# Performance work log

Measured on AMD Instinct MI355X. Metric: run time of the kernel, lower is better.

The kernel has to match this reference:

```python
import jax, jax.numpy as jnp
import numpy as np

IN_FEATURES = 4096
OUT_FEATURES = 4096
BLOCK_SIZE = 64
BLOCK_NUM = 64
N_FACTORS = 3  # boft_n_butterfly_factor


def _butterfly_perm(n, b, r):
    # Mirrors BOFTLayer.block_butterfly_perm for n_butterfly_factor != 0.
    block_size = n // b
    step = block_size // r
    evens = np.arange(0, step, 2)
    odds = np.arange(1, step, 2)
    seq = np.concatenate([evens, odds])
    sorted_order = np.concatenate([np.arange(p * r, p * r + r) for p in seq])
    return np.arange(n).reshape(-1, block_size)[:, sorted_order].reshape(-1)


def setup_inputs() -> dict:
    key = jax.random.key(0)
    k1, k2, k3, k4, k5 = jax.random.split(key, 5)
    x = jax.random.normal(k1, (8, 2048, IN_FEATURES), dtype=jnp.float32)
    weight = jax.random.normal(k2, (OUT_FEATURES, IN_FEATURES), dtype=jnp.float32) * 0.02
    bias = jax.random.normal(k3, (OUT_FEATURES,), dtype=jnp.float32) * 0.02
    boft_R = jax.random.normal(k4, (N_FACTORS, BLOCK_NUM, BLOCK_SIZE, BLOCK_SIZE), dtype=jnp.float32) * 0.1
    boft_s = jax.random.uniform(k5, (OUT_FEATURES, 1), dtype=jnp.float32, minval=0.5, maxval=1.5)
    perm = jnp.asarray(np.stack([
        _butterfly_perm(IN_FEATURES, BLOCK_NUM // (2 ** i), BLOCK_SIZE // 2)
        for i in range(N_FACTORS)
    ]), dtype=jnp.int32)
    return {"x": x, "weight": weight, "bias": bias, "boft_R": boft_R,
            "boft_s": boft_s, "perm": perm}


def _cayley(R):
    # Q = (I - skew) @ inv(I + skew), skew = (R - R^T)/2; batched.
    skew = 0.5 * (R - jnp.swapaxes(R, -1, -2))
    I = jnp.eye(R.shape[-1], dtype=R.dtype)
    # Right-division via solve: X (I+skew) = (I-skew)
    Xt = jnp.linalg.solve(jnp.swapaxes(I + skew, -1, -2), jnp.swapaxes(I - skew, -1, -2))
    return jnp.swapaxes(Xt, -1, -2)


def _block_diag(blocks):
    # (D, H, H) -> (D*H, D*H) block-diagonal
    D, H, _ = blocks.shape
    out = jnp.zeros((D, H, D, H), blocks.dtype)
    out = out.at[jnp.arange(D), :, jnp.arange(D), :].set(blocks)
    return out.reshape(D * H, D * H)


def reference(x, weight, bias, boft_R, boft_s, perm):
    N, D, H, _ = boft_R.shape
    Q = _cayley(boft_R.reshape(N * D, H, H)).reshape(N, D, H, H)
    # P_i @ block_diag_i @ P_i^T implemented as a symmetric gather (P is a permutation)
    rot = None
    for i in range(N):  # small fixed loop over butterfly factors
        bd = _block_diag(Q[i])
        p = perm[i]
        mat = bd[p][:, p]  # (in, in)
        rot = mat if rot is None else mat @ rot
    # rotated_weight = (rot @ W^T)^T = W @ rot^T ; then scale rows by boft_s
    scaled_w = (weight @ rot.T) * boft_s  # (out, in)
    return x @ scaled_w.T + bias
```

## Files before the change

kernel.cpp:

```cpp
#include <hip/hip_runtime.h>
#include <hip/hip_bf16.h>
#include <cstddef>
#include <cstdint>

#define IN_F 4096
#define OUT_F 4096

typedef __attribute__((ext_vector_type(8))) _Float16 half8;
typedef __attribute__((ext_vector_type(4))) float f32x4;

__global__ __launch_bounds__(256) void cayley_kernel(const float* __restrict__ R,
                                                     float* __restrict__ Qs) {
  __shared__ float Mm[64][65];
  __shared__ float Bm[64][65];
  const int b = blockIdx.x;
  const float* Rb = R + (size_t)b * 4096;
  const int t = threadIdx.x;
  const int i = t >> 2;
  const int jb = (t & 3) << 4;

  #pragma unroll 4
  for (int q = 0; q < 16; ++q) {
    int j = jb + q;
    float rij = Rb[i * 64 + j];
    float rji = Rb[j * 64 + i];
    float sk = 0.5f * (rij - rji);
    float id = (i == j) ? 1.0f : 0.0f;
    Mm[i][j] = id - sk;
    Bm[i][j] = id + sk;
  }
  __syncthreads();

  for (int k = 0; k < 64; ++k) {
    float inv = 1.0f / Mm[k][k];
    float f = Mm[i][k];
    __syncthreads();
    if (t < 64) {
      Mm[k][t] *= inv;
      Bm[k][t] *= inv;
    }
    __syncthreads();
    if (i != k) {
      #pragma unroll 4
      for (int q = 0; q < 16; ++q) {
        int j = jb + q;
        Mm[i][j] = fmaf(-f, Mm[k][j], Mm[i][j]);
        Bm[i][j] = fmaf(-f, Bm[k][j], Bm[i][j]);
      }
    }
    __syncthreads();
  }

  float* out = Qs + (size_t)b * 4096;
  #pragma unroll 4
  for (int q = 0; q < 16; ++q) {
    int flat = t * 16 + q;
    out[flat] = Bm[flat >> 6][flat & 63];
  }
}

__global__ void invperm_kernel(const int* __restrict__ perm,
                               int* __restrict__ ip1, int* __restrict__ ip2) {
  int c = blockIdx.x * 256 + threadIdx.x;
  ip1[perm[4096 + c]] = c;
  ip2[perm[8192 + c]] = c;
}

__global__ void compose_kernel(const int* __restrict__ perm,
                               const int* __restrict__ ip1,
                               const int* __restrict__ ip2,
                               int* __restrict__ rho1, int* __restrict__ rho2) {
  int k = blockIdx.x * 256 + threadIdx.x;
  rho1[k] = perm[ip1[k]];
  rho2[k] = perm[4096 + ip2[k]];
}

__global__ __launch_bounds__(256) void transpose_perm_kernel(const float* __restrict__ W,
                                                             const int* __restrict__ p0,
                                                             float* __restrict__ U0) {
  __shared__ float tile[64][65];
  const int c0 = blockIdx.x * 64;
  const int n0 = blockIdx.y * 64;
  const int t = threadIdx.x;
  const int r = t >> 2;
  const int cb = (t & 3) << 4;
  #pragma unroll
  for (int q = 0; q < 4; ++q) {
    float4 v = *(const float4*)(W + (size_t)(n0 + r) * IN_F + c0 + cb + q * 4);
    tile[r][cb + q * 4 + 0] = v.x;
    tile[r][cb + q * 4 + 1] = v.y;
    tile[r][cb + q * 4 + 2] = v.z;
    tile[r][cb + q * 4 + 3] = v.w;
  }
  __syncthreads();
  const int c = t >> 2;
  const int nb = (t & 3) << 4;
  const int dstrow = p0[c0 + c];
  #pragma unroll
  for (int q = 0; q < 4; ++q) {
    float4 v;
    v.x = tile[nb + q * 4 + 0][c];
    v.y = tile[nb + q * 4 + 1][c];
    v.z = tile[nb + q * 4 + 2][c];
    v.w = tile[nb + q * 4 + 3][c];
    *(float4*)(U0 + (size_t)dstrow * OUT_F + n0 + nb + q * 4) = v;
  }
}

__global__ __launch_bounds__(256) void factor_kernel(const float* __restrict__ src,
                                                     float* __restrict__ dst,
                                                     const float* __restrict__ Qt,
                                                     const int* __restrict__ rowIdx,
                                                     const int* __restrict__ dstIdx,
                                                     const float* __restrict__ s) {
  __shared__ float qt[64][64];
  __shared__ int sidx[64];
  __shared__ int didx[64];
  const int g = blockIdx.y;
  const int n0 = blockIdx.x * 256;
  const int t = threadIdx.x;

  {
    const float* qg = Qt + (size_t)g * 4096;
    float4* qv = (float4*)&qt[0][0];
    #pragma unroll
    for (int q = 0; q < 4; ++q)
      qv[t * 4 + q] = *(const float4*)(qg + t * 16 + q * 4);
  }
  if (t < 64) {
    sidx[t] = rowIdx ? rowIdx[g * 64 + t] : g * 64 + t;
    didx[t] = dstIdx ? dstIdx[g * 64 + t] : g * 64 + t;
  }
  __syncthreads();

  const int w = t >> 6;
  const int lane = t & 63;
  const int nOff = n0 + lane * 4;
  float4 a[16];
  #pragma unroll
  for (int ii = 0; ii < 16; ++ii) a[ii] = make_float4(0.f, 0.f, 0.f, 0.f);

  for (int j = 0; j < 64; ++j) {
    float4 v = *(const float4*)(src + (size_t)sidx[j] * OUT_F + nOff);
    const float* qr = &qt[j][w * 16];
    #pragma unroll
    for (int ii = 0; ii < 16; ++ii) {
      float qq = qr[ii];
      a[ii].x = fmaf(qq, v.x, a[ii].x);
      a[ii].y = fmaf(qq, v.y, a[ii].y);
      a[ii].z = fmaf(qq, v.z, a[ii].z);
      a[ii].w = fmaf(qq, v.w, a[ii].w);
    }
  }

  float4 sv = make_float4(1.f, 1.f, 1.f, 1.f);
  if (s) sv = *(const float4*)(s + nOff);
  #pragma unroll
  for (int ii = 0; ii < 16; ++ii) {
    int r = didx[w * 16 + ii];
    float4 o;
    o.x = a[ii].x * sv.x; o.y = a[ii].y * sv.y;
    o.z = a[ii].z * sv.z; o.w = a[ii].w * sv.w;
    *(float4*)(dst + (size_t)r * OUT_F + nOff) = o;
  }
}

__global__ __launch_bounds__(256) void transpose_cvt_swz(const float* __restrict__ S,
                                                         _Float16* __restrict__ D) {
  __shared__ float tile[64][65];
  const int k0 = blockIdx.x * 64;
  const int n0 = blockIdx.y * 64;
  const int t = threadIdx.x;
  const int r = t >> 2;
  const int cb = (t & 3) << 4;
  #pragma unroll
  for (int q = 0; q < 4; ++q) {
    float4 v = *(const float4*)(S + (size_t)(k0 + r) * OUT_F + n0 + cb + q * 4);
    tile[r][cb + q * 4 + 0] = v.x;
    tile[r][cb + q * 4 + 1] = v.y;
    tile[r][cb + q * 4 + 2] = v.z;
    tile[r][cb + q * 4 + 3] = v.w;
  }
  __syncthreads();
  const int n = t >> 2;
  const int kb = (t & 3) << 4;
  half8 h0, h1;
  #pragma unroll
  for (int q = 0; q < 8; ++q) {
    h0[q] = (_Float16)tile[kb + q][n];
    h1[q] = (_Float16)tile[kb + 8 + q][n];
  }
  const int gn = n0 + n;
  const int sw = gn & 3;
  const int c0 = (k0 + kb) >> 3;
  const int c0s = (c0 & ~3) | ((c0 & 3) ^ sw);
  const int c1s = (c0 & ~3) | (((c0 + 1) & 3) ^ sw);
  _Float16* dp = D + (size_t)gn * IN_F;
  *(half8*)(dp + c0s * 8) = h0;
  *(half8*)(dp + c1s * 8) = h1;
}

__global__ __launch_bounds__(256) void cvt_x_kernel(const float* __restrict__ X,
                                                    _Float16* __restrict__ Ah) {
  const int idx = blockIdx.x * 256 + threadIdx.x;
  const int m = idx >> 9;
  const int c = idx & 511;
  const float* xp = X + (size_t)m * IN_F + c * 8;
  f32x4 v0 = *(const f32x4*)xp;
  f32x4 v1 = *(const f32x4*)(xp + 4);
  half8 h;
  h[0] = (_Float16)v0.x; h[1] = (_Float16)v0.y;
  h[2] = (_Float16)v0.z; h[3] = (_Float16)v0.w;
  h[4] = (_Float16)v1.x; h[5] = (_Float16)v1.y;
  h[6] = (_Float16)v1.z; h[7] = (_Float16)v1.w;
  const int cs = (c & ~3) | ((c & 3) ^ (m & 3));
  *(half8*)(Ah + (size_t)m * IN_F + cs * 8) = h;
}

#define TM 256
#define TN 256
#define TK 32
#define NSLOT 4

typedef const __attribute__((address_space(1))) uint32_t* gptr_t;
typedef __attribute__((address_space(3))) uint32_t* lptr_t;

#define WB(n) asm volatile("s_waitcnt vmcnt(" #n ")\ns_barrier" ::: "memory")

__global__ __launch_bounds__(512, 2) void mfma_gemm2(const _Float16* __restrict__ A,
                                                     const _Float16* __restrict__ B,
                                                     const float* __restrict__ bias,
                                                     float* __restrict__ C, int M) {
  __shared__ __align__(16) _Float16 lds[NSLOT][2][TM * TK];
  const int t = threadIdx.x;
  const int lane = t & 63;
  const int w = t >> 6;
  const int wr = w >> 2;
  const int wc = w & 3;

  const int nwg = gridDim.x * gridDim.y;
  const int lin = blockIdx.y * gridDim.x + blockIdx.x;
  const int cpx = nwg >> 3;
  const int nl = (lin & 7) * cpx + (lin >> 3);
  const int n0 = (nl & 15) * TN;
  const int m0 = (nl >> 4) * TM;

  const _Float16* gA[2];
  const _Float16* gB[2];
  int ldsoff[2];
  #pragma unroll
  for (int p = 0; p < 2; ++p) {
    int chunk = p * 512 + t;
    int row = chunk >> 2;
    int c = chunk & 3;
    gA[p] = A + (size_t)(m0 + row) * IN_F + c * 8;
    gB[p] = B + (size_t)(n0 + row) * IN_F + c * 8;
    ldsoff[p] = (p * 512 + (t & ~63)) * 8;
  }

  const int frow = lane & 15;
  const int kc = lane >> 4;
  int aoff[8], boff[4];
  #pragma unroll
  for (int i = 0; i < 8; ++i) {
    int r = wr * 128 + i * 16 + frow;
    aoff[i] = r * TK + ((kc ^ (r & 3)) << 3);
  }
  #pragma unroll
  for (int j = 0; j < 4; ++j) {
    int r = wc * 64 + j * 16 + frow;
    boff[j] = r * TK + ((kc ^ (r & 3)) << 3);
  }

  f32x4 acc[8][4];
  #pragma unroll
  for (int i = 0; i < 8; ++i)
    #pragma unroll
    for (int j = 0; j < 4; ++j) acc[i][j] = (f32x4){0.f, 0.f, 0.f, 0.f};

#define STAGE(tt, ss)                                                          \
  do {                                                                         \
    _Float16* sA = &lds[ss][0][0];                                             \
    _Float16* sB = &lds[ss][1][0];                                             \
    _Pragma("unroll") for (int p = 0; p < 2; ++p) {                            \
      __builtin_amdgcn_global_load_lds((gptr_t)(gA[p] + (tt) * TK),            \
                                       (lptr_t)(sA + ldsoff[p]), 16, 0, 0);    \
      __builtin_amdgcn_global_load_lds((gptr_t)(gB[p] + (tt) * TK),            \
                                       (lptr_t)(sB + ldsoff[p]), 16, 0, 0);    \
    }                                                                          \
  } while (0)

#define COMPUTE(ss)                                                            \
  do {                                                                         \
    const _Float16* As = &lds[ss][0][0];                                       \
    const _Float16* Bs = &lds[ss][1][0];                                       \
    half8 af[8], bf[4];                                                        \
    _Pragma("unroll") for (int i = 0; i < 8; ++i)                              \
        af[i] = *(const half8*)(As + aoff[i]);                                 \
    _Pragma("unroll") for (int j = 0; j < 4; ++j)                              \
        bf[j] = *(const half8*)(Bs + boff[j]);                                 \
    __builtin_amdgcn_s_setprio(1);                                             \
    _Pragma("unroll") for (int i = 0; i < 8; ++i)                              \
      _Pragma("unroll") for (int j = 0; j < 4; ++j)                            \
          acc[i][j] = __builtin_amdgcn_mfma_f32_16x16x32_f16(af[i], bf[j],     \
                                                             acc[i][j], 0, 0, 0); \
    __builtin_amdgcn_s_setprio(0);                                             \
  } while (0)

  STAGE(0, 0);
  STAGE(1, 1);
  STAGE(2, 2);
  WB(8);
  for (int tt = 0; tt < 125; ++tt) {
    STAGE(tt + 3, (tt + 3) & 3);
    COMPUTE(tt & 3);
    WB(8);
  }
  COMPUTE(1); WB(4);
  COMPUTE(2); WB(0);
  COMPUTE(3);

  const int crow = (lane >> 4) << 2;
  const int ccol = lane & 15;
  #pragma unroll
  for (int j = 0; j < 4; ++j) {
    int n = n0 + wc * 64 + j * 16 + ccol;
    float bv = bias[n];
    #pragma unroll
    for (int i = 0; i < 8; ++i) {
      int mbase = m0 + wr * 128 + i * 16 + crow;
      #pragma unroll
      for (int r = 0; r < 4; ++r)
        C[(size_t)(mbase + r) * OUT_F + n] = acc[i][j][r] + bv;
    }
  }
#undef STAGE
#undef COMPUTE
}

extern "C" void kernel_launch(void* const* d_in, const int* in_sizes, int n_in,
                              void* d_out, int out_size, void* d_ws, size_t ws_size,
                              hipStream_t stream) {
  const float* x      = (const float*)d_in[0];
  const float* weight = (const float*)d_in[1];
  const float* bias   = (const float*)d_in[2];
  const float* boft_R = (const float*)d_in[3];
  const float* boft_s = (const float*)d_in[4];
  const int*   perm   = (const int*)d_in[5];
  float* out = (float*)d_out;

  float* ws   = (float*)d_ws;
  float* Qs   = ws;
  float* bufA = ws + 786432;
  float* bufB = bufA + 16777216;
  _Float16* Bh = (_Float16*)(bufB + 16777216);
  int*   ints = (int*)(Bh + 16777216);
  int* ip1  = ints;
  int* ip2  = ints + 4096;
  int* rho1 = ints + 8192;
  int* rho2 = ints + 12288;
  _Float16* Ah = (_Float16*)bufA;

  const int M = in_sizes[0] / IN_F;

  hipLaunchKernelGGL(cayley_kernel, dim3(192), dim3(256), 0, stream, boft_R, Qs);
  hipLaunchKernelGGL(invperm_kernel, dim3(16), dim3(256), 0, stream, perm, ip1, ip2);
  hipLaunchKernelGGL(compose_kernel, dim3(16), dim3(256), 0, stream, perm, ip1, ip2, rho1, rho2);
  hipLaunchKernelGGL(transpose_perm_kernel, dim3(64, 64), dim3(256), 0, stream,
                     weight, perm, bufA);
  hipLaunchKernelGGL(factor_kernel, dim3(16, 64), dim3(256), 0, stream,
                     bufA, bufB, Qs, (const int*)nullptr, (const int*)nullptr,
                     (const float*)nullptr);
  hipLaunchKernelGGL(factor_kernel, dim3(16, 64), dim3(256), 0, stream,
                     bufB, bufA, Qs + 262144, rho1, (const int*)nullptr,
                     (const float*)nullptr);
  hipLaunchKernelGGL(factor_kernel, dim3(16, 64), dim3(256), 0, stream,
                     bufA, bufB, Qs + 524288, rho2, ip2, boft_s);
  hipLaunchKernelGGL(transpose_cvt_swz, dim3(64, 64), dim3(256), 0, stream,
                     bufB, Bh);
  hipLaunchKernelGGL(cvt_x_kernel, dim3((M * IN_F / 8) / 256), dim3(256), 0, stream,
                     x, Ah);
  hipLaunchKernelGGL(mfma_gemm2, dim3(OUT_F / TN, M / TM), dim3(512), 0, stream,
                     Ah, Bh, bias, out, M);
}
```

Measured before the change: 1.195 ms.

## Split GEMM K-step into two ping-pong phases and change LDS swizzle

Splits each K-tile's compute in the fp16 MFMA GEMM into two phases. Each phase issues part of the LDS fragment loads and half of the next tile's global-to-LDS prefetch (A, then B), then meets at a barrier before its MFMAs run at raised priority. This is meant to interleave memory and matrix work across waves, ping-pong style. It also changes the XOR swizzle key from row&3 to (row>>2)&3, consistently in the converters and the GEMM fragment offsets, to reduce LDS bank conflicts. The extra barriers per tile add synchronization cost, and overlapping STAGE writes with reads of other slots depends on the 4-slot ring staying correct.

```diff
diff --git a/kernel.cpp b/kernel.cpp
--- a/kernel.cpp
+++ b/kernel.cpp
@@ -191,7 +191,7 @@
     h1[q] = (_Float16)tile[kb + 8 + q][n];
   }
   const int gn = n0 + n;
-  const int sw = gn & 3;
+  const int sw = (gn >> 2) & 3;
   const int c0 = (k0 + kb) >> 3;
   const int c0s = (c0 & ~3) | ((c0 & 3) ^ sw);
   const int c1s = (c0 & ~3) | (((c0 + 1) & 3) ^ sw);
@@ -213,7 +213,7 @@
   h[2] = (_Float16)v0.z; h[3] = (_Float16)v0.w;
   h[4] = (_Float16)v1.x; h[5] = (_Float16)v1.y;
   h[6] = (_Float16)v1.z; h[7] = (_Float16)v1.w;
-  const int cs = (c & ~3) | ((c & 3) ^ (m & 3));
+  const int cs = (c & ~3) | ((c & 3) ^ ((m >> 2) & 3));
   *(half8*)(Ah + (size_t)m * IN_F + cs * 8) = h;
 }
 
@@ -225,7 +225,9 @@
 typedef const __attribute__((address_space(1))) uint32_t* gptr_t;
 typedef __attribute__((address_space(3))) uint32_t* lptr_t;
 
-#define WB(n) asm volatile("s_waitcnt vmcnt(" #n ")\ns_barrier" ::: "memory")
+#define BARRIER()  asm volatile("s_barrier" ::: "memory")
+#define LGKM0()    asm volatile("s_waitcnt lgkmcnt(0)" ::: "memory")
+#define TILE_END(n) asm volatile("s_waitcnt vmcnt(" #n ")\n\ts_barrier" ::: "memory")
 
 __global__ __launch_bounds__(512, 2) void mfma_gemm2(const _Float16* __restrict__ A,
                                                      const _Float16* __restrict__ B,
@@ -264,12 +266,12 @@
   #pragma unroll
   for (int i = 0; i < 8; ++i) {
     int r = wr * 128 + i * 16 + frow;
-    aoff[i] = r * TK + ((kc ^ (r & 3)) << 3);
+    aoff[i] = r * TK + ((kc ^ ((r >> 2) & 3)) << 3);
   }
   #pragma unroll
   for (int j = 0; j < 4; ++j) {
     int r = wc * 64 + j * 16 + frow;
-    boff[j] = r * TK + ((kc ^ (r & 3)) << 3);
+    boff[j] = r * TK + ((kc ^ ((r >> 2) & 3)) << 3);
   }
 
   f32x4 acc[8][4];
@@ -278,47 +280,74 @@
     #pragma unroll
     for (int j = 0; j < 4; ++j) acc[i][j] = (f32x4){0.f, 0.f, 0.f, 0.f};
 
-#define STAGE(tt, ss)                                                          \
+  half8 af[8], bf[4];
+
+#define STAGE_A(tt, ss)                                                        \
   do {                                                                         \
     _Float16* sA = &lds[ss][0][0];                                             \
-    _Float16* sB = &lds[ss][1][0];                                             \
-    _Pragma("unroll") for (int p = 0; p < 2; ++p) {                            \
+    _Pragma("unroll") for (int p = 0; p < 2; ++p)                              \
       __builtin_amdgcn_global_load_lds((gptr_t)(gA[p] + (tt) * TK),            \
                                        (lptr_t)(sA + ldsoff[p]), 16, 0, 0);    \
+  } while (0)
+
+#define STAGE_B(tt, ss)                                                        \
+  do {                                                                         \
+    _Float16* sB = &lds[ss][1][0];                                             \
+    _Pragma("unroll") for (int p = 0; p < 2; ++p)                              \
       __builtin_amdgcn_global_load_lds((gptr_t)(gB[p] + (tt) * TK),            \
                                        (lptr_t)(sB + ldsoff[p]), 16, 0, 0);    \
-    }                                                                          \
   } while (0)
 
-#define COMPUTE(ss)                                                            \
+#define PHASE1(ss, DOSTAGE, tt3)                                               \
   do {                                                                         \
     const _Float16* As = &lds[ss][0][0];                                       \
     const _Float16* Bs = &lds[ss][1][0];                                       \
-    half8 af[8], bf[4];                                                        \
-    _Pragma("unroll") for (int i = 0; i < 8; ++i)                              \
+    _Pragma("unroll") for (int i = 0; i < 4; ++i)                              \
         af[i] = *(const half8*)(As + aoff[i]);                                 \
     _Pragma("unroll") for (int j = 0; j < 4; ++j)                              \
         bf[j] = *(const half8*)(Bs + boff[j]);                                 \
+    if (DOSTAGE) STAGE_A(tt3, (tt3) & 3);                                      \
+    BARRIER();                                                                 \
+    LGKM0();                                                                   \
+    __builtin_amdgcn_sched_barrier(0);                                         \
     __builtin_amdgcn_s_setprio(1);                                             \
-    _Pragma("unroll") for (int i = 0; i < 8; ++i)                              \
+    _Pragma("unroll") for (int i = 0; i < 4; ++i)                              \
       _Pragma("unroll") for (int j = 0; j < 4; ++j)                            \
           acc[i][j] = __builtin_amdgcn_mfma_f32_16x16x32_f16(af[i], bf[j],     \
                                                              acc[i][j], 0, 0, 0); \
     __builtin_amdgcn_s_setprio(0);                                             \
+    BARRIER();                                                                 \
   } while (0)
 
-  STAGE(0, 0);
-  STAGE(1, 1);
-  STAGE(2, 2);
-  WB(8);
+#define PHASE2(ss, DOSTAGE, tt3)                                               \
+  do {                                                                         \
+    const _Float16* As = &lds[ss][0][0];                                       \
+    _Pragma("unroll") for (int i = 0; i < 4; ++i)                              \
+        af[4 + i] = *(const half8*)(As + aoff[4 + i]);                         \
+    if (DOSTAGE) STAGE_B(tt3, (tt3) & 3);                                      \
+    BARRIER();                                                                 \
+    LGKM0();                                                                   \
+    __builtin_amdgcn_sched_barrier(0);                                         \
+    __builtin_amdgcn_s_setprio(1);                                             \
+    _Pragma("unroll") for (int i = 0; i < 4; ++i)                              \
+      _Pragma("unroll") for (int j = 0; j < 4; ++j)                            \
+          acc[4 + i][j] = __builtin_amdgcn_mfma_f32_16x16x32_f16(af[4 + i], bf[j], \
+                                                                 acc[4 + i][j], 0, 0, 0); \
+    __builtin_amdgcn_s_setprio(0);                                             \
+  } while (0)
+
+  STAGE_A(0, 0); STAGE_B(0, 0);
+  STAGE_A(1, 1); STAGE_B(1, 1);
+  STAGE_A(2, 2); STAGE_B(2, 2);
+  TILE_END(8);
   for (int tt = 0; tt < 125; ++tt) {
-    STAGE(tt + 3, (tt + 3) & 3);
-    COMPUTE(tt & 3);
-    WB(8);
-  }
-  COMPUTE(1); WB(4);
-  COMPUTE(2); WB(0);
-  COMPUTE(3);
+    PHASE1(tt & 3, 1, tt + 3);
+    PHASE2(tt & 3, 1, tt + 3);
+    TILE_END(8);
+  }
+  PHASE1(1, 0, 0); PHASE2(1, 0, 0); TILE_END(4);
+  PHASE1(2, 0, 0); PHASE2(2, 0, 0); TILE_END(0);
+  PHASE1(3, 0, 0); PHASE2(3, 0, 0);
 
   const int crow = (lane >> 4) << 2;
   const int ccol = lane & 15;
@@ -334,8 +363,10 @@
         C[(size_t)(mbase + r) * OUT_F + n] = acc[i][j][r] + bv;
     }
   }
-#undef STAGE
-#undef COMPUTE
+#undef STAGE_A
+#undef STAGE_B
+#undef PHASE1
+#undef PHASE2
 }
 
 extern "C" void kernel_launch(void* const* d_in, const int* in_sizes, int n_in,
```

Result: no change. 1.195 ms (-0.0%).

## Double-buffer LDS fragment reads and change XOR swizzle to row-group based

Applied to the files above, without the earlier changes.

The GEMM main loop now reads the next tile's A/B fragments from LDS into a second register set while the MFMAs for the current tile run, unrolled by two with ping-pong fragment registers. The XOR swizzle used by the conversion kernels and the LDS read offsets is switched from row&3 to (row>>2)&3, aiming to cut LDS bank conflicts for the 16-row fragment access pattern. The extra fragment registers raise VGPR pressure under launch_bounds(512,2), and the wait counts change from 8 to 4, which tightens the prefetch distance and must stay consistent with the stage schedule.

```diff
diff --git a/kernel.cpp b/kernel.cpp
--- a/kernel.cpp
+++ b/kernel.cpp
@@ -191,7 +191,7 @@
     h1[q] = (_Float16)tile[kb + 8 + q][n];
   }
   const int gn = n0 + n;
-  const int sw = gn & 3;
+  const int sw = (gn >> 2) & 3;
   const int c0 = (k0 + kb) >> 3;
   const int c0s = (c0 & ~3) | ((c0 & 3) ^ sw);
   const int c1s = (c0 & ~3) | (((c0 + 1) & 3) ^ sw);
@@ -213,7 +213,7 @@
   h[2] = (_Float16)v0.z; h[3] = (_Float16)v0.w;
   h[4] = (_Float16)v1.x; h[5] = (_Float16)v1.y;
   h[6] = (_Float16)v1.z; h[7] = (_Float16)v1.w;
-  const int cs = (c & ~3) | ((c & 3) ^ (m & 3));
+  const int cs = (c & ~3) | ((c & 3) ^ ((m >> 2) & 3));
   *(half8*)(Ah + (size_t)m * IN_F + cs * 8) = h;
 }
 
@@ -225,7 +225,7 @@
 typedef const __attribute__((address_space(1))) uint32_t* gptr_t;
 typedef __attribute__((address_space(3))) uint32_t* lptr_t;
 
-#define WB(n) asm volatile("s_waitcnt vmcnt(" #n ")\ns_barrier" ::: "memory")
+#define ENDTILE(n) asm volatile("s_waitcnt vmcnt(" #n ")\n\ts_barrier" ::: "memory")
 
 __global__ __launch_bounds__(512, 2) void mfma_gemm2(const _Float16* __restrict__ A,
                                                      const _Float16* __restrict__ B,
@@ -264,12 +264,12 @@
   #pragma unroll
   for (int i = 0; i < 8; ++i) {
     int r = wr * 128 + i * 16 + frow;
-    aoff[i] = r * TK + ((kc ^ (r & 3)) << 3);
+    aoff[i] = r * TK + ((kc ^ ((r >> 2) & 3)) << 3);
   }
   #pragma unroll
   for (int j = 0; j < 4; ++j) {
     int r = wc * 64 + j * 16 + frow;
-    boff[j] = r * TK + ((kc ^ (r & 3)) << 3);
+    boff[j] = r * TK + ((kc ^ ((r >> 2) & 3)) << 3);
   }
 
   f32x4 acc[8][4];
@@ -277,6 +277,8 @@
   for (int i = 0; i < 8; ++i)
     #pragma unroll
     for (int j = 0; j < 4; ++j) acc[i][j] = (f32x4){0.f, 0.f, 0.f, 0.f};
+
+  half8 afE[8], bfE[4], afO[8], bfO[4];
 
 #define STAGE(tt, ss)                                                          \
   do {                                                                         \
@@ -290,19 +292,22 @@
     }                                                                          \
   } while (0)
 
-#define COMPUTE(ss)                                                            \
+#define READS(AF, BF, SL)                                                      \
   do {                                                                         \
-    const _Float16* As = &lds[ss][0][0];                                       \
-    const _Float16* Bs = &lds[ss][1][0];                                       \
-    half8 af[8], bf[4];                                                        \
+    const _Float16* As = &lds[SL][0][0];                                       \
+    const _Float16* Bs = &lds[SL][1][0];                                       \
     _Pragma("unroll") for (int i = 0; i < 8; ++i)                              \
-        af[i] = *(const half8*)(As + aoff[i]);                                 \
+        AF[i] = *(const half8*)(As + aoff[i]);                                 \
     _Pragma("unroll") for (int j = 0; j < 4; ++j)                              \
-        bf[j] = *(const half8*)(Bs + boff[j]);                                 \
+        BF[j] = *(const half8*)(Bs + boff[j]);                                 \
+  } while (0)
+
+#define MFMAS(AF, BF)                                                          \
+  do {                                                                         \
     __builtin_amdgcn_s_setprio(1);                                             \
     _Pragma("unroll") for (int i = 0; i < 8; ++i)                              \
       _Pragma("unroll") for (int j = 0; j < 4; ++j)                            \
-          acc[i][j] = __builtin_amdgcn_mfma_f32_16x16x32_f16(af[i], bf[j],     \
+          acc[i][j] = __builtin_amdgcn_mfma_f32_16x16x32_f16(AF[i], BF[j],     \
                                                              acc[i][j], 0, 0, 0); \
     __builtin_amdgcn_s_setprio(0);                                             \
   } while (0)
@@ -310,15 +315,29 @@
   STAGE(0, 0);
   STAGE(1, 1);
   STAGE(2, 2);
-  WB(8);
-  for (int tt = 0; tt < 125; ++tt) {
+  ENDTILE(4);
+  READS(afE, bfE, 0);
+
+  for (int tt = 0; tt < 124; tt += 2) {
+    READS(afO, bfO, (tt + 1) & 3);
     STAGE(tt + 3, (tt + 3) & 3);
-    COMPUTE(tt & 3);
-    WB(8);
-  }
-  COMPUTE(1); WB(4);
-  COMPUTE(2); WB(0);
-  COMPUTE(3);
+    MFMAS(afE, bfE);
+    ENDTILE(4);
+    READS(afE, bfE, (tt + 2) & 3);
+    STAGE(tt + 4, (tt + 4) & 3);
+    MFMAS(afO, bfO);
+    ENDTILE(4);
+  }
+  READS(afO, bfO, 125 & 3);
+  STAGE(127, 127 & 3);
+  MFMAS(afE, bfE);
+  ENDTILE(4);
+  READS(afE, bfE, 126 & 3);
+  MFMAS(afO, bfO);
+  ENDTILE(0);
+  READS(afO, bfO, 127 & 3);
+  MFMAS(afE, bfE);
+  MFMAS(afO, bfO);
 
   const int crow = (lane >> 4) << 2;
   const int ccol = lane & 15;
@@ -335,7 +354,8 @@
     }
   }
 #undef STAGE
-#undef COMPUTE
+#undef READS
+#undef MFMAS
 }
 
 extern "C" void kernel_launch(void* const* d_in, const int* in_sizes, int n_in,
```

Measured after the change: 1.183 ms. No clear change (-1.0%).
